# Kernel tuning notes

Hardware: AMD Instinct MI355X
Metric: run time of the kernel (lower is better)

The kernel has to match this reference:

```python
import jax, jax.numpy as jnp
import numpy as np

N = 10000
E = 160000
D_IN = 512
D_OUT = 512


def setup_inputs() -> dict:
    key = jax.random.key(0)
    k1, k2, k3, k4, k5 = jax.random.split(key, 5)
    x = jax.random.normal(k1, (N, D_IN), dtype=jnp.float32)
    edge_index = jax.random.randint(k2, (2, E), 0, N, dtype=jnp.int64)
    edge_attr = jax.random.uniform(k3, (E,), dtype=jnp.float32)
    W = jax.random.normal(k4, (D_IN, D_OUT), dtype=jnp.float32) * 0.05
    b = jax.random.normal(k5, (D_OUT,), dtype=jnp.float32) * 0.05
    return {"x": x, "edge_index": edge_index, "edge_attr": edge_attr, "W": W, "b": b}


def reference(x, edge_index, edge_attr, W, b):
    # PyG GCNConv with normalize=True, add_self_loops=True, edge_weight=edge_attr.
    n = x.shape[0]
    row, col = edge_index[0], edge_index[1]
    # Add self loops with weight 1.0 (fill_value=1.)
    loop = jnp.arange(n, dtype=edge_index.dtype)
    row_f = jnp.concatenate([row, loop])      # [E+N] source nodes
    col_f = jnp.concatenate([col, loop])      # [E+N] target nodes
    ew = jnp.concatenate([edge_attr, jnp.ones((n,), dtype=edge_attr.dtype)])
    # Symmetric normalization: deg computed over target index (col)
    deg = jax.ops.segment_sum(ew, col_f, num_segments=n)
    dinv = jnp.where(deg > 0, jax.lax.rsqrt(deg), 0.0)
    norm = dinv[row_f] * ew * dinv[col_f]     # [E+N]
    # Linear transform (no bias inside lin), then gather-scale-scatter
    h = x @ W                                  # [N, D_OUT]
    msg = h[row_f] * norm[:, None]             # [E+N, D_OUT]
    out = jax.ops.segment_sum(msg, col_f, num_segments=n)
    return out + b
```

## Files before the change

### kernel.cpp

```cpp
#include <hip/hip_runtime.h>

#define NN 10000
#define EE 160000
#define DD 512
#define CAP 128

typedef float floatx4 __attribute__((ext_vector_type(4)));
typedef short short8 __attribute__((ext_vector_type(8)));

#define AS3(p) ((__attribute__((address_space(3))) void*)(p))
#define AS1(p) ((const __attribute__((address_space(1))) void*)(p))

static __device__ __forceinline__ unsigned short f2bf(float f) {
    unsigned int u = __float_as_uint(f);
    unsigned int r = (u + 0x7fffu + ((u >> 16) & 1u)) >> 16;
    return (unsigned short)r;
}
static __device__ __forceinline__ float bflo(unsigned int u) {
    return __uint_as_float(u << 16);
}
static __device__ __forceinline__ float bfhi(unsigned int u) {
    return __uint_as_float(u & 0xffff0000u);
}


#define XB_BLOCKS 5000
#define WT_BLOCKS 256
#define ACC_BLOCKS 625

__global__ __launch_bounds__(256) void k_prep(const float* __restrict__ x,
                                              const float* __restrict__ W,
                                              const int* __restrict__ col,
                                              const float* __restrict__ ew,
                                              unsigned short* __restrict__ xb,
                                              unsigned short* __restrict__ wtb,
                                              float* __restrict__ deg) {
    const int b = blockIdx.x;
    const int tid = threadIdx.x;
    if (b < XB_BLOCKS) {
        int gid = b * 256 + tid;
        float4 v = *(const float4*)&x[(size_t)gid * 4];
        unsigned int p0 = (unsigned int)f2bf(v.x) | ((unsigned int)f2bf(v.y) << 16);
        unsigned int p1 = (unsigned int)f2bf(v.z) | ((unsigned int)f2bf(v.w) << 16);
        *(uint2*)&xb[(size_t)gid * 4] = make_uint2(p0, p1);
    } else if (b < XB_BLOCKS + WT_BLOCKS) {
        __shared__ float T[32][33];
        int idx = b - XB_BLOCKS;
        int bi = idx & 15;
        int bj = idx >> 4;
        int r0 = tid >> 5;
        int cc = tid & 31;
        #pragma unroll
        for (int k = 0; k < 4; k++) {
            int r = r0 + k * 8;
            T[r][cc] = W[(size_t)(bi * 32 + r) * DD + bj * 32 + cc];
        }
        __syncthreads();
        #pragma unroll
        for (int k = 0; k < 4; k++) {
            int r = r0 + k * 8;
            wtb[(size_t)(bj * 32 + r) * DD + bi * 32 + cc] = f2bf(T[cc][r]);
        }
    } else {
        int e = (b - XB_BLOCKS - WT_BLOCKS) * 256 + tid;
        atomicAdd(&deg[col[e]], ew[e]);
    }
}


__global__ void k_place(const int* __restrict__ row, const int* __restrict__ col,
                        const float* __restrict__ ew, const float* __restrict__ deg,
                        int* __restrict__ cursor,
                        int* __restrict__ erow, float* __restrict__ enorm) {
    int e = blockIdx.x * 256 + threadIdx.x;
    if (e < EE) {
        int r = row[e];
        int t = col[e];
        float dr = rsqrtf(deg[r] + 1.0f);
        float dt = rsqrtf(deg[t] + 1.0f);
        float nm = dr * ew[e] * dt;
        int p = atomicAdd(&cursor[t], 1);
        if (p < CAP) {
            erow[t * CAP + p] = r;
            enorm[t * CAP + p] = nm;
        }
    }
}


__global__ __launch_bounds__(256) void k_gemm_mfma(const unsigned short* __restrict__ xb,
                                                   const unsigned short* __restrict__ wtb,
                                                   unsigned short* __restrict__ hb) {
    __shared__ unsigned short As[128 * 32];
    __shared__ unsigned short Bs[128 * 32];

    const int tid = threadIdx.x;
    const int wave = tid >> 6;
    const int lane = tid & 63;

    const int bm = blockIdx.x * 128;
    const int bn = blockIdx.y * 128;

    const int wm = (wave >> 1) * 64;
    const int wn = (wave & 1) * 64;

    const int fm = lane & 15;
    const int kb = (lane >> 4) * 8;

    floatx4 acc[4][4];
    #pragma unroll
    for (int i = 0; i < 4; i++)
        #pragma unroll
        for (int j = 0; j < 4; j++)
            acc[i][j] = (floatx4){0.f, 0.f, 0.f, 0.f};

    const int srow = lane >> 2;
    const int scol = (lane & 3) * 8;

    for (int k0 = 0; k0 < DD; k0 += 32) {
        #pragma unroll
        for (int cc = 0; cc < 2; cc++) {
            int c = wave + cc * 4;
            int r = c * 16 + srow;
            int gr = bm + r; if (gr > NN - 1) gr = NN - 1;
            __builtin_amdgcn_global_load_lds(AS1(xb + (size_t)gr * DD + k0 + scol),
                                             AS3(&As[c * 512]), 16, 0, 0);
            int nr = bn + r;
            __builtin_amdgcn_global_load_lds(AS1(wtb + (size_t)nr * DD + k0 + scol),
                                             AS3(&Bs[c * 512]), 16, 0, 0);
        }
        __syncthreads();

        short8 af[4], bfr[4];
        #pragma unroll
        for (int mi = 0; mi < 4; mi++)
            af[mi] = *(const short8*)&As[(wm + mi * 16 + fm) * 32 + kb];
        #pragma unroll
        for (int ni = 0; ni < 4; ni++)
            bfr[ni] = *(const short8*)&Bs[(wn + ni * 16 + fm) * 32 + kb];

        #pragma unroll
        for (int mi = 0; mi < 4; mi++)
            #pragma unroll
            for (int ni = 0; ni < 4; ni++)
                acc[mi][ni] = __builtin_amdgcn_mfma_f32_16x16x32_bf16(af[mi], bfr[ni], acc[mi][ni], 0, 0, 0);

        __syncthreads();
    }

    #pragma unroll
    for (int mi = 0; mi < 4; mi++) {
        #pragma unroll
        for (int ni = 0; ni < 4; ni++) {
            int colg = bn + wn + ni * 16 + (lane & 15);
            int rbase = bm + wm + mi * 16 + (lane >> 4) * 4;
            #pragma unroll
            for (int j = 0; j < 4; j++) {
                int rg = rbase + j;
                if (rg < NN) hb[(size_t)rg * DD + colg] = f2bf(acc[mi][ni][j]);
            }
        }
    }
}


__global__ __launch_bounds__(128) void k_aggregate(const int* __restrict__ cursor,
                                                   const int* __restrict__ erow,
                                                   const float* __restrict__ enorm,
                                                   const unsigned short* __restrict__ hb,
                                                   const float* __restrict__ deg,
                                                   const float* __restrict__ bias,
                                                   float* __restrict__ out) {
    const int h = threadIdx.x >> 6;
    const int t = threadIdx.x & 63;
    const int i = blockIdx.x * 2 + h;
    const int c = t << 3;

    __shared__ int   s_r[2][CAP];
    __shared__ float s_w[2][CAP];

    int cnt = cursor[i];
    if (cnt > CAP) cnt = CAP;
    const int base = i * CAP;
    if (t < cnt)      { s_r[h][t]      = erow[base + t];      s_w[h][t]      = enorm[base + t]; }
    if (t + 64 < cnt) { s_r[h][t + 64] = erow[base + t + 64]; s_w[h][t + 64] = enorm[base + t + 64]; }
    __syncthreads();

    float acc[8] = {0.f, 0.f, 0.f, 0.f, 0.f, 0.f, 0.f, 0.f};

    int j = 0;
    for (; j + 2 <= cnt; j += 2) {
        int r0 = s_r[h][j];     float w0 = s_w[h][j];
        int r1 = s_r[h][j + 1]; float w1 = s_w[h][j + 1];
        uint4 p0 = *(const uint4*)&hb[(size_t)r0 * DD + c];
        uint4 p1 = *(const uint4*)&hb[(size_t)r1 * DD + c];
        acc[0] += bflo(p0.x) * w0; acc[1] += bfhi(p0.x) * w0;
        acc[2] += bflo(p0.y) * w0; acc[3] += bfhi(p0.y) * w0;
        acc[4] += bflo(p0.z) * w0; acc[5] += bfhi(p0.z) * w0;
        acc[6] += bflo(p0.w) * w0; acc[7] += bfhi(p0.w) * w0;
        acc[0] += bflo(p1.x) * w1; acc[1] += bfhi(p1.x) * w1;
        acc[2] += bflo(p1.y) * w1; acc[3] += bfhi(p1.y) * w1;
        acc[4] += bflo(p1.z) * w1; acc[5] += bfhi(p1.z) * w1;
        acc[6] += bflo(p1.w) * w1; acc[7] += bfhi(p1.w) * w1;
    }
    if (j < cnt) {
        int r0 = s_r[h][j]; float w0 = s_w[h][j];
        uint4 p0 = *(const uint4*)&hb[(size_t)r0 * DD + c];
        acc[0] += bflo(p0.x) * w0; acc[1] += bfhi(p0.x) * w0;
        acc[2] += bflo(p0.y) * w0; acc[3] += bfhi(p0.y) * w0;
        acc[4] += bflo(p0.z) * w0; acc[5] += bfhi(p0.z) * w0;
        acc[6] += bflo(p0.w) * w0; acc[7] += bfhi(p0.w) * w0;
    }

    float s = 1.0f / (deg[i] + 1.0f);
    uint4 hv = *(const uint4*)&hb[(size_t)i * DD + c];
    float4 bv0 = *(const float4*)&bias[c];
    float4 bv1 = *(const float4*)&bias[c + 4];
    float4 o0, o1;
    o0.x = acc[0] + bflo(hv.x) * s + bv0.x;
    o0.y = acc[1] + bfhi(hv.x) * s + bv0.y;
    o0.z = acc[2] + bflo(hv.y) * s + bv0.z;
    o0.w = acc[3] + bfhi(hv.y) * s + bv0.w;
    o1.x = acc[4] + bflo(hv.z) * s + bv1.x;
    o1.y = acc[5] + bfhi(hv.z) * s + bv1.y;
    o1.z = acc[6] + bflo(hv.w) * s + bv1.z;
    o1.w = acc[7] + bfhi(hv.w) * s + bv1.w;
    *(float4*)&out[(size_t)i * DD + c] = o0;
    *(float4*)&out[(size_t)i * DD + c + 4] = o1;
}

extern "C" void kernel_launch(void* const* d_in, const int* in_sizes, int n_in,
                              void* d_out, int out_size, void* d_ws, size_t ws_size,
                              hipStream_t stream) {
    const float* x  = (const float*)d_in[0];
    const int*   ei = (const int*)d_in[1];
    const float* ea = (const float*)d_in[2];
    const float* W  = (const float*)d_in[3];
    const float* b  = (const float*)d_in[4];
    float* out = (float*)d_out;

    char* ws = (char*)d_ws;
    unsigned short* hb   = (unsigned short*)ws;
    unsigned short* xb   = (unsigned short*)(ws + 10240000);
    unsigned short* wtb  = (unsigned short*)(ws + 20480000);
    float* deg    = (float*)(ws + 21004288);
    int*   cursor = (int*)  (ws + 21045248);
    int*   erow   = (int*)  (ws + 21086208);
    float* enorm  = (float*)(ws + 26206208);

    const int* row = ei;
    const int* col = ei + EE;

    hipMemsetAsync(deg, 0, 81920, stream);

    k_prep<<<XB_BLOCKS + WT_BLOCKS + ACC_BLOCKS, 256, 0, stream>>>(x, W, col, ea, xb, wtb, deg);

    dim3 ggrid((NN + 127) / 128, DD / 128);
    k_gemm_mfma<<<ggrid, 256, 0, stream>>>(xb, wtb, hb);

    k_place<<<(EE + 255) / 256, 256, 0, stream>>>(row, col, ea, deg, cursor, erow, enorm);

    k_aggregate<<<NN / 2, 128, 0, stream>>>(cursor, erow, enorm, hb, deg, b, out);
}
```

Before: 146.3 us.

## Fold degree normalization into GEMM epilogue and merge edge placement into prep

The per-edge normalization dinv[r]*w*dinv[t] is factored so that dinv of the source row is applied in the GEMM epilogue and dinv of the target is applied once per output row in aggregation. Since the per-edge norm no longer depends on the final degree, edge bucketing moves into the prep kernel alongside the degree atomics, which removes the separate k_place launch. Row index and weight are packed into a uint2 so each bucket entry is a single load. The change relies on the memset to zero deg and cursor, adds one rsqrt per row in the GEMM, and shifts the bf16 rounding point in the computation.

```diff
diff --git a/kernel.cpp b/kernel.cpp
--- a/kernel.cpp
+++ b/kernel.cpp
@@ -26,15 +26,18 @@
 
 #define XB_BLOCKS 5000
 #define WT_BLOCKS 256
-#define ACC_BLOCKS 625
+#define EDGE_BLOCKS 625
 
 __global__ __launch_bounds__(256) void k_prep(const float* __restrict__ x,
                                               const float* __restrict__ W,
+                                              const int* __restrict__ row,
                                               const int* __restrict__ col,
                                               const float* __restrict__ ew,
                                               unsigned short* __restrict__ xb,
                                               unsigned short* __restrict__ wtb,
-                                              float* __restrict__ deg) {
+                                              float* __restrict__ deg,
+                                              int* __restrict__ cursor,
+                                              uint2* __restrict__ erw) {
     const int b = blockIdx.x;
     const int tid = threadIdx.x;
     if (b < XB_BLOCKS) {
@@ -63,33 +66,19 @@
         }
     } else {
         int e = (b - XB_BLOCKS - WT_BLOCKS) * 256 + tid;
-        atomicAdd(&deg[col[e]], ew[e]);
-    }
-}
-
-
-__global__ void k_place(const int* __restrict__ row, const int* __restrict__ col,
-                        const float* __restrict__ ew, const float* __restrict__ deg,
-                        int* __restrict__ cursor,
-                        int* __restrict__ erow, float* __restrict__ enorm) {
-    int e = blockIdx.x * 256 + threadIdx.x;
-    if (e < EE) {
         int r = row[e];
         int t = col[e];
-        float dr = rsqrtf(deg[r] + 1.0f);
-        float dt = rsqrtf(deg[t] + 1.0f);
-        float nm = dr * ew[e] * dt;
+        float w = ew[e];
+        atomicAdd(&deg[t], w);
         int p = atomicAdd(&cursor[t], 1);
-        if (p < CAP) {
-            erow[t * CAP + p] = r;
-            enorm[t * CAP + p] = nm;
-        }
+        if (p < CAP) erw[t * CAP + p] = make_uint2((unsigned int)r, __float_as_uint(w));
     }
 }
 
 
 __global__ __launch_bounds__(256) void k_gemm_mfma(const unsigned short* __restrict__ xb,
                                                    const unsigned short* __restrict__ wtb,
+                                                   const float* __restrict__ deg,
                                                    unsigned short* __restrict__ hb) {
     __shared__ unsigned short As[128 * 32];
     __shared__ unsigned short Bs[128 * 32];
@@ -148,6 +137,17 @@
         __syncthreads();
     }
 
+    float dv[4][4];
+    #pragma unroll
+    for (int mi = 0; mi < 4; mi++) {
+        int rbase = bm + wm + mi * 16 + (lane >> 4) * 4;
+        #pragma unroll
+        for (int j = 0; j < 4; j++) {
+            int rg = rbase + j; if (rg > NN - 1) rg = NN - 1;
+            dv[mi][j] = rsqrtf(deg[rg] + 1.0f);
+        }
+    }
+
     #pragma unroll
     for (int mi = 0; mi < 4; mi++) {
         #pragma unroll
@@ -157,7 +157,7 @@
             #pragma unroll
             for (int j = 0; j < 4; j++) {
                 int rg = rbase + j;
-                if (rg < NN) hb[(size_t)rg * DD + colg] = f2bf(acc[mi][ni][j]);
+                if (rg < NN) hb[(size_t)rg * DD + colg] = f2bf(acc[mi][ni][j] * dv[mi][j]);
             }
         }
     }
@@ -165,8 +165,7 @@
 
 
 __global__ __launch_bounds__(128) void k_aggregate(const int* __restrict__ cursor,
-                                                   const int* __restrict__ erow,
-                                                   const float* __restrict__ enorm,
+                                                   const uint2* __restrict__ erw,
                                                    const unsigned short* __restrict__ hb,
                                                    const float* __restrict__ deg,
                                                    const float* __restrict__ bias,
@@ -181,9 +180,9 @@
 
     int cnt = cursor[i];
     if (cnt > CAP) cnt = CAP;
-    const int base = i * CAP;
-    if (t < cnt)      { s_r[h][t]      = erow[base + t];      s_w[h][t]      = enorm[base + t]; }
-    if (t + 64 < cnt) { s_r[h][t + 64] = erow[base + t + 64]; s_w[h][t + 64] = enorm[base + t + 64]; }
+    const uint2* bkt = erw + (size_t)i * CAP;
+    if (t < cnt)      { uint2 p = bkt[t];      s_r[h][t]      = (int)p.x; s_w[h][t]      = __uint_as_float(p.y); }
+    if (t + 64 < cnt) { uint2 p = bkt[t + 64]; s_r[h][t + 64] = (int)p.x; s_w[h][t + 64] = __uint_as_float(p.y); }
     __syncthreads();
 
     float acc[8] = {0.f, 0.f, 0.f, 0.f, 0.f, 0.f, 0.f, 0.f};
@@ -212,19 +211,19 @@
         acc[6] += bflo(p0.w) * w0; acc[7] += bfhi(p0.w) * w0;
     }
 
-    float s = 1.0f / (deg[i] + 1.0f);
+    float dv = rsqrtf(deg[i] + 1.0f);
     uint4 hv = *(const uint4*)&hb[(size_t)i * DD + c];
     float4 bv0 = *(const float4*)&bias[c];
     float4 bv1 = *(const float4*)&bias[c + 4];
     float4 o0, o1;
-    o0.x = acc[0] + bflo(hv.x) * s + bv0.x;
-    o0.y = acc[1] + bfhi(hv.x) * s + bv0.y;
-    o0.z = acc[2] + bflo(hv.y) * s + bv0.z;
-    o0.w = acc[3] + bfhi(hv.y) * s + bv0.w;
-    o1.x = acc[4] + bflo(hv.z) * s + bv1.x;
-    o1.y = acc[5] + bfhi(hv.z) * s + bv1.y;
-    o1.z = acc[6] + bflo(hv.w) * s + bv1.z;
-    o1.w = acc[7] + bfhi(hv.w) * s + bv1.w;
+    o0.x = (acc[0] + bflo(hv.x)) * dv + bv0.x;
+    o0.y = (acc[1] + bfhi(hv.x)) * dv + bv0.y;
+    o0.z = (acc[2] + bflo(hv.y)) * dv + bv0.z;
+    o0.w = (acc[3] + bfhi(hv.y)) * dv + bv0.w;
+    o1.x = (acc[4] + bflo(hv.z)) * dv + bv1.x;
+    o1.y = (acc[5] + bfhi(hv.z)) * dv + bv1.y;
+    o1.z = (acc[6] + bflo(hv.w)) * dv + bv1.z;
+    o1.w = (acc[7] + bfhi(hv.w)) * dv + bv1.w;
     *(float4*)&out[(size_t)i * DD + c] = o0;
     *(float4*)&out[(size_t)i * DD + c + 4] = o1;
 }
@@ -245,20 +244,18 @@
     unsigned short* wtb  = (unsigned short*)(ws + 20480000);
     float* deg    = (float*)(ws + 21004288);
     int*   cursor = (int*)  (ws + 21045248);
-    int*   erow   = (int*)  (ws + 21086208);
-    float* enorm  = (float*)(ws + 26206208);
+    uint2* erw    = (uint2*)(ws + 21086208);
 
     const int* row = ei;
     const int* col = ei + EE;
 
     hipMemsetAsync(deg, 0, 81920, stream);
 
-    k_prep<<<XB_BLOCKS + WT_BLOCKS + ACC_BLOCKS, 256, 0, stream>>>(x, W, col, ea, xb, wtb, deg);
+    k_prep<<<XB_BLOCKS + WT_BLOCKS + EDGE_BLOCKS, 256, 0, stream>>>(x, W, row, col, ea,
+                                                                    xb, wtb, deg, cursor, erw);
 
     dim3 ggrid((NN + 127) / 128, DD / 128);
-    k_gemm_mfma<<<ggrid, 256, 0, stream>>>(xb, wtb, hb);
-
-    k_place<<<(EE + 255) / 256, 256, 0, stream>>>(row, col, ea, deg, cursor, erow, enorm);
-
-    k_aggregate<<<NN / 2, 128, 0, stream>>>(cursor, erow, enorm, hb, deg, b, out);
-}
+    k_gemm_mfma<<<ggrid, 256, 0, stream>>>(xb, wtb, deg, hb);
+
+    k_aggregate<<<NN / 2, 128, 0, stream>>>(cursor, erw, hb, deg, b, out);
+}
```

Result: faster. 140.8 us (-3.7%).
